# Kernel optimization log

Measured on AMD Instinct MI355X. Metric: run time of the kernel, lower is better.

The kernel has to match this reference:

```python
import jax, jax.numpy as jnp
import numpy as np

B, C, NC, H, W = 8, 128, 19, 128, 256
EPS = 1e-5


def ste_round(x):
    # straight-through-estimator round (Brevitas-style)
    return x + jax.lax.stop_gradient(jnp.round(x) - x)


def quant_weight(w):
    # int4 symmetric per-output-channel fake-quant: levels [-7, 7]
    s = jnp.maximum(jnp.max(jnp.abs(w), axis=(1, 2, 3), keepdims=True) / 7.0, 1e-8)
    wq = jnp.clip(ste_round(w / s), -7.0, 7.0) * s
    return wq, s


def quant_relu(x, s):
    # ReLU + uint4 fake-quant with learned per-tensor scale: levels [0, 15]
    return jnp.clip(ste_round(x / s), 0.0, 15.0) * s


def batchnorm(x, g, b, m, v):
    scale = (g / jnp.sqrt(v + EPS))[None, :, None, None]
    return (x - m[None, :, None, None]) * scale + b[None, :, None, None]


def dwconv3x3(x, w):
    # w: [C,1,3,3], groups=C
    return jax.lax.conv_general_dilated(
        x, w, window_strides=(1, 1), padding=((1, 1), (1, 1)),
        dimension_numbers=('NCHW', 'OIHW', 'NCHW'),
        feature_group_count=x.shape[1])


def pwconv(x, w):
    # 1x1 conv as einsum; w: [O,I,1,1]
    return jnp.einsum('bchw,oc->bohw', x, w[:, :, 0, 0])


def dsconv(x, dw_w, bn1, s1, pw_w, bn2, s2):
    wq, _ = quant_weight(dw_w)
    x = dwconv3x3(x, wq)
    x = batchnorm(x, *bn1)
    x = quant_relu(x, s1)
    wq, _ = quant_weight(pw_w)
    x = pwconv(x, wq)
    x = batchnorm(x, *bn2)
    x = quant_relu(x, s2)
    return x


def setup_inputs() -> dict:
    key = jax.random.key(0)
    ks = jax.random.split(key, 16)
    d = {}
    d['x'] = jax.random.normal(ks[0], (B, C, H, W), dtype=jnp.float32)
    d['dw1_w'] = jax.random.normal(ks[1], (C, 1, 3, 3), dtype=jnp.float32) * 0.1
    d['pw1_w'] = jax.random.normal(ks[2], (C, C, 1, 1), dtype=jnp.float32) * 0.05
    d['dw2_w'] = jax.random.normal(ks[3], (C, 1, 3, 3), dtype=jnp.float32) * 0.1
    d['pw2_w'] = jax.random.normal(ks[4], (C, C, 1, 1), dtype=jnp.float32) * 0.05
    d['cls_w'] = jax.random.normal(ks[5], (NC, C, 1, 1), dtype=jnp.float32) * 0.05
    d['cls_b'] = jax.random.normal(ks[6], (NC,), dtype=jnp.float32) * 0.1
    for i, kk in zip(range(1, 5), ks[7:11]):
        sub = jax.random.split(kk, 4)
        d[f'bn{i}_g'] = 1.0 + 0.1 * jax.random.normal(sub[0], (C,), dtype=jnp.float32)
        d[f'bn{i}_b'] = 0.1 * jax.random.normal(sub[1], (C,), dtype=jnp.float32)
        d[f'bn{i}_m'] = 0.1 * jax.random.normal(sub[2], (C,), dtype=jnp.float32)
        d[f'bn{i}_v'] = jax.random.uniform(sub[3], (C,), dtype=jnp.float32, minval=0.5, maxval=1.5)
    d['s_a1'] = jnp.float32(0.2)
    d['s_a2'] = jnp.float32(0.2)
    d['s_a3'] = jnp.float32(0.2)
    d['s_a4'] = jnp.float32(0.2)
    return d


def reference(x, dw1_w, pw1_w, dw2_w, pw2_w, cls_w, cls_b,
              bn1_g, bn1_b, bn1_m, bn1_v,
              bn2_g, bn2_b, bn2_m, bn2_v,
              bn3_g, bn3_b, bn3_m, bn3_v,
              bn4_g, bn4_b, bn4_m, bn4_v,
              s_a1, s_a2, s_a3, s_a4):
    x = dsconv(x, dw1_w, (bn1_g, bn1_b, bn1_m, bn1_v), s_a1,
               pw1_w, (bn2_g, bn2_b, bn2_m, bn2_v), s_a2)
    x = dsconv(x, dw2_w, (bn3_g, bn3_b, bn3_m, bn3_v), s_a3,
               pw2_w, (bn4_g, bn4_b, bn4_m, bn4_v), s_a4)
    # QuantDropout p=0.1 is identity in eval mode
    wq, sw = quant_weight(cls_w)
    # IntBias: bias quantized with scale = act_scale * weight_scale (per out channel)
    sb = s_a4 * sw[:, 0, 0, 0]
    bq = ste_round(cls_b / sb) * sb
    out = pwconv(x, wq) + bq[None, :, None, None]
    return out
```

## Files before the change

kernel.cpp:

```cpp
#include <hip/hip_runtime.h>

typedef __attribute__((ext_vector_type(4))) float f32x4;
typedef __attribute__((ext_vector_type(8))) short bf16x8;
typedef __attribute__((ext_vector_type(2))) unsigned int u32x2;
typedef __attribute__((ext_vector_type(4))) unsigned int u32x4;

#define EPSV 1e-5f

#define OFF_BUFA 0u
#define OFF_BUFB 33554432u
#define OFF_T    67108864u
#define OFF_WQ1  (OFF_T + 0u)
#define OFF_R3F  (OFF_T + 6144u)
#define OFF_CST3 (OFF_T + 10752u)
#define OFF_CST1 (OFF_T + 12800u)
#define OFF_R2BF (OFF_T + 14848u)
#define OFF_CST2 (OFF_T + 47616u)
#define OFF_R4BF (OFF_T + 49664u)
#define OFF_CST4 (OFF_T + 82432u)
#define OFF_R5BF (OFF_T + 84480u)
#define OFF_CST5 (OFF_T + 92672u)

struct PArgs {
  const float *dw1, *pw1, *dw2, *pw2, *clsw, *clsb;
  const float *g1, *b1, *m1, *v1;
  const float *g2, *b2, *m2, *v2;
  const float *g3, *b3, *m3, *v3;
  const float *g4, *b4, *m4, *v4;
  const float *s1, *s2, *s3, *s4;
};

__device__ __forceinline__ unsigned short f2bf(float f) {
  return (unsigned short)(__builtin_bit_cast(unsigned int, f) >> 16);
}
__device__ __forceinline__ float clip7(float r) { return fminf(fmaxf(r, -7.f), 7.f); }

__device__ __forceinline__ unsigned int qstep(float a, f32x4 c, float s) {
  float t = (a * c.x - c.z) * c.y + c.w;
  float u = t / s;
  float k = fminf(fmaxf(rintf(u), 0.f), 15.f);
  return (unsigned int)k;
}

__device__ __forceinline__ void cvt2(unsigned int d, unsigned int &lo, unsigned int &hi) {
  float f0 = (float)(d & 0xffu);
  float f1 = (float)((d >> 8) & 0xffu);
  float f2 = (float)((d >> 16) & 0xffu);
  float f3 = (float)(d >> 24);
  lo = (__builtin_bit_cast(unsigned int, f0) >> 16) | (__builtin_bit_cast(unsigned int, f1) & 0xffff0000u);
  hi = (__builtin_bit_cast(unsigned int, f2) >> 16) | (__builtin_bit_cast(unsigned int, f3) & 0xffff0000u);
}

__device__ __forceinline__ float wmax16(float v) {
  #pragma unroll
  for (int s = 1; s < 16; s <<= 1) v = fmaxf(v, __shfl_xor(v, s));
  return v;
}
__device__ __forceinline__ float wmax64(float v) {
  #pragma unroll
  for (int s = 1; s < 64; s <<= 1) v = fmaxf(v, __shfl_xor(v, s));
  return v;
}

__global__ __launch_bounds__(64) void prep_kernel(PArgs P, char* __restrict__ ws) {
  int bi = blockIdx.x, l = threadIdx.x;
  float* wq1 = (float*)(ws + OFF_WQ1);
  float* r3f = (float*)(ws + OFF_R3F);
  f32x4* cst1 = (f32x4*)(ws + OFF_CST1);
  f32x4* cst2 = (f32x4*)(ws + OFF_CST2);
  f32x4* cst3 = (f32x4*)(ws + OFF_CST3);
  f32x4* cst4 = (f32x4*)(ws + OFF_CST4);
  unsigned short* r2 = (unsigned short*)(ws + OFF_R2BF);
  unsigned short* r4 = (unsigned short*)(ws + OFF_R4BF);
  unsigned short* r5 = (unsigned short*)(ws + OFF_R5BF);
  float2* cst5 = (float2*)(ws + OFF_CST5);

  if (bi < 128) {
    int c = bi;
    float w = (l < 9) ? P.dw1[c * 9 + l] : 0.f;
    float mx = wmax16(fabsf(w));
    float sq = fmaxf(mx / 7.0f, 1e-8f);
    if (l < 9) wq1[c * 12 + l] = clip7(rintf(w / sq)) * sq;
    if (l == 0) {
      float sc = P.g1[c] / sqrtf(P.v1[c] + EPSV);
      cst1[c] = f32x4{1.f, sc, P.m1[c], P.b1[c]};
    }
  } else if (bi < 256) {
    int o = bi - 128;
    float w0 = P.pw1[o * 128 + l], w1 = P.pw1[o * 128 + 64 + l];
    float mx = wmax64(fmaxf(fabsf(w0), fabsf(w1)));
    float sq = fmaxf(mx / 7.0f, 1e-8f);
    r2[o * 128 + l]      = f2bf(clip7(rintf(w0 / sq)));
    r2[o * 128 + 64 + l] = f2bf(clip7(rintf(w1 / sq)));
    if (l == 0) {
      float sc = P.g2[o] / sqrtf(P.v2[o] + EPSV);
      cst2[o] = f32x4{P.s1[0] * sq, sc, P.m2[o], P.b2[o]};
    }
  } else if (bi < 384) {
    int c = bi - 256;
    float w = (l < 9) ? P.dw2[c * 9 + l] : 0.f;
    float mx = wmax16(fabsf(w));
    float sq = fmaxf(mx / 7.0f, 1e-8f);
    if (l < 9) r3f[l * 128 + c] = clip7(rintf(w / sq));
    if (l == 0) {
      float sc = P.g3[c] / sqrtf(P.v3[c] + EPSV);
      cst3[c] = f32x4{P.s2[0] * sq, sc, P.m3[c], P.b3[c]};
    }
  } else if (bi < 512) {
    int o = bi - 384;
    float w0 = P.pw2[o * 128 + l], w1 = P.pw2[o * 128 + 64 + l];
    float mx = wmax64(fmaxf(fabsf(w0), fabsf(w1)));
    float sq = fmaxf(mx / 7.0f, 1e-8f);
    r4[o * 128 + l]      = f2bf(clip7(rintf(w0 / sq)));
    r4[o * 128 + 64 + l] = f2bf(clip7(rintf(w1 / sq)));
    if (l == 0) {
      float sc = P.g4[o] / sqrtf(P.v4[o] + EPSV);
      cst4[o] = f32x4{P.s3[0] * sq, sc, P.m4[o], P.b4[o]};
    }
  } else {
    int o = bi - 512;
    if (o < 19) {
      float w0 = P.clsw[o * 128 + l], w1 = P.clsw[o * 128 + 64 + l];
      float mx = wmax64(fmaxf(fabsf(w0), fabsf(w1)));
      float sq = fmaxf(mx / 7.0f, 1e-8f);
      r5[o * 128 + l]      = f2bf(clip7(rintf(w0 / sq)));
      r5[o * 128 + 64 + l] = f2bf(clip7(rintf(w1 / sq)));
      if (l == 0) {
        float A5 = P.s4[0] * sq;
        float bq = rintf(P.clsb[o] / A5) * A5;
        cst5[o] = make_float2(A5, bq);
      }
    } else {
      r5[o * 128 + l] = 0; r5[o * 128 + 64 + l] = 0;
      if (l == 0) cst5[o] = make_float2(0.f, 0.f);
    }
  }
}

__global__ __launch_bounds__(512) void dwA_kernel(const float* __restrict__ x,
                                                  char* __restrict__ ws,
                                                  const float* __restrict__ s1p) {
  int bid = blockIdx.x;
  int b = bid & 7, c = bid >> 3;
  int tid = threadIdx.x;
  int wq = tid & 63, wv = tid >> 6;
  int w0 = wq << 2;
  int h0 = wv << 4;
  const float* wp = (const float*)(ws + OFF_WQ1) + c * 12;
  float k0 = wp[0], k1 = wp[1], k2 = wp[2], k3 = wp[3], k4 = wp[4],
        k5 = wp[5], k6 = wp[6], k7 = wp[7], k8 = wp[8];
  f32x4 cs = ((const f32x4*)(ws + OFF_CST1))[c];
  float s_act = *s1p;
  const float* plane = x + (((size_t)((b << 7) | c)) << 15);
  unsigned char* oplane = (unsigned char*)(ws + OFF_BUFB) + (((size_t)((b << 7) | c)) << 15);

  f32x4 vm = {0.f, 0.f, 0.f, 0.f};
  if (h0 > 0) vm = *(const f32x4*)(plane + ((h0 - 1) << 8) + w0);
  f32x4 v0 = *(const f32x4*)(plane + (h0 << 8) + w0);
  f32x4 vp = *(const f32x4*)(plane + ((h0 + 1) << 8) + w0);
  float lm = __shfl_up(vm.w, 1), l0 = __shfl_up(v0.w, 1), lp = __shfl_up(vp.w, 1);
  float rm = __shfl_down(vm.x, 1), r0 = __shfl_down(v0.x, 1), rp = __shfl_down(vp.x, 1);
  if (wq == 0)  { lm = 0.f; l0 = 0.f; lp = 0.f; }
  if (wq == 63) { rm = 0.f; r0 = 0.f; rp = 0.f; }

  #pragma unroll 4
  for (int i = 0; i < 16; i++) {
    int h = h0 + i;
    float y0 = 0.f, y1 = 0.f, y2 = 0.f, y3 = 0.f;
    y0 = fmaf(lm,   k0, y0); y0 = fmaf(vm.x, k1, y0); y0 = fmaf(vm.y, k2, y0);
    y1 = fmaf(vm.x, k0, y1); y1 = fmaf(vm.y, k1, y1); y1 = fmaf(vm.z, k2, y1);
    y2 = fmaf(vm.y, k0, y2); y2 = fmaf(vm.z, k1, y2); y2 = fmaf(vm.w, k2, y2);
    y3 = fmaf(vm.z, k0, y3); y3 = fmaf(vm.w, k1, y3); y3 = fmaf(rm,   k2, y3);

    y0 = fmaf(l0,   k3, y0); y0 = fmaf(v0.x, k4, y0); y0 = fmaf(v0.y, k5, y0);
    y1 = fmaf(v0.x, k3, y1); y1 = fmaf(v0.y, k4, y1); y1 = fmaf(v0.z, k5, y1);
    y2 = fmaf(v0.y, k3, y2); y2 = fmaf(v0.z, k4, y2); y2 = fmaf(v0.w, k5, y2);
    y3 = fmaf(v0.z, k3, y3); y3 = fmaf(v0.w, k4, y3); y3 = fmaf(r0,   k5, y3);

    y0 = fmaf(lp,   k6, y0); y0 = fmaf(vp.x, k7, y0); y0 = fmaf(vp.y, k8, y0);
    y1 = fmaf(vp.x, k6, y1); y1 = fmaf(vp.y, k7, y1); y1 = fmaf(vp.z, k8, y1);
    y2 = fmaf(vp.y, k6, y2); y2 = fmaf(vp.z, k7, y2); y2 = fmaf(vp.w, k8, y2);
    y3 = fmaf(vp.z, k6, y3); y3 = fmaf(vp.w, k7, y3); y3 = fmaf(rp,   k8, y3);

    unsigned int pk = qstep(y0, cs, s_act) | (qstep(y1, cs, s_act) << 8) |
                      (qstep(y2, cs, s_act) << 16) | (qstep(y3, cs, s_act) << 24);
    *(unsigned int*)(oplane + (h << 8) + w0) = pk;

    vm = v0; lm = l0; rm = r0;
    v0 = vp; l0 = lp; r0 = rp;
    f32x4 nv = {0.f, 0.f, 0.f, 0.f};
    if (i < 15 && h + 2 < 128) nv = *(const f32x4*)(plane + ((h + 2) << 8) + w0);
    vp = nv;
    float nl = __shfl_up(nv.w, 1), nr = __shfl_down(nv.x, 1);
    if (wq == 0)  nl = 0.f;
    if (wq == 63) nr = 0.f;
    lp = nl; rp = nr;
  }
}

__global__ __launch_bounds__(256) void pwn_kernel(const unsigned char* __restrict__ in,
                                                  unsigned char* __restrict__ out,
                                                  const unsigned short* __restrict__ rbf,
                                                  const f32x4* __restrict__ cst,
                                                  const float* __restrict__ sp) {
  __shared__ unsigned char lds[32768];
  int tid = threadIdx.x;
  int p0 = blockIdx.x << 7;
  int b_img = p0 >> 15, loc0 = p0 & 32767;
  {
    int pb = tid & 7, cq = tid >> 3;
    int c4 = cq << 2;
    int kc = cq >> 3, lgr = (cq >> 1) & 3, half = cq & 1;
    const unsigned char* ib = in + (((size_t)(b_img << 7)) << 15) + loc0 + (pb << 4);
    u32x4 t0 = *(const u32x4*)(ib + ((size_t)(c4 + 0) << 15));
    u32x4 t1 = *(const u32x4*)(ib + ((size_t)(c4 + 1) << 15));
    u32x4 t2 = *(const u32x4*)(ib + ((size_t)(c4 + 2) << 15));
    u32x4 t3 = *(const u32x4*)(ib + ((size_t)(c4 + 3) << 15));
    int swz = (pb & 7) << 4;
    #pragma unroll
    for (int s = 0; s < 16; s++) {
      int wrd = s >> 2, sh8 = (s & 3) << 3;
      unsigned int chw = ((t0[wrd] >> sh8) & 0xffu)
                       | (((t1[wrd] >> sh8) & 0xffu) << 8)
                       | (((t2[wrd] >> sh8) & 0xffu) << 16)
                       | (((t3[wrd] >> sh8) & 0xffu) << 24);
      unsigned int lo, hi;
      cvt2(chw, lo, hi);
      int ad = ((((((pb << 2) + kc) << 6) | s | (lgr << 4)) << 4) + (half << 3)) ^ swz;
      *(u32x2*)(lds + ad) = u32x2{lo, hi};
    }
  }
  __syncthreads();
  int l = tid & 63, wv = tid >> 6;
  int ob = wv << 5;
  bf16x8 af[2][4];
  #pragma unroll
  for (int ot = 0; ot < 2; ot++)
    #pragma unroll
    for (int kc = 0; kc < 4; kc++) {
      int o = ob + (ot << 4) + (l & 15);
      int k = (kc << 5) + ((l >> 4) << 3);
      af[ot][kc] = *(const bf16x8*)(rbf + o * 128 + k);
    }
  f32x4 acc[2][8];
  #pragma unroll
  for (int ot = 0; ot < 2; ot++)
    #pragma unroll
    for (int pt = 0; pt < 8; pt++) acc[ot][pt] = f32x4{0.f, 0.f, 0.f, 0.f};
  #pragma unroll
  for (int kc = 0; kc < 4; kc++) {
    bf16x8 bb[8];
    #pragma unroll
    for (int pt = 0; pt < 8; pt++)
      bb[pt] = *(const bf16x8*)(lds + (((((((pt << 2) + kc) << 6)) + l) << 4) ^ ((pt & 7) << 4)));
    #pragma unroll
    for (int ot = 0; ot < 2; ot++)
      #pragma unroll
      for (int pt = 0; pt < 8; pt++)
        acc[ot][pt] = __builtin_amdgcn_mfma_f32_16x16x32_bf16(af[ot][kc], bb[pt], acc[ot][pt], 0, 0, 0);
  }
  float s_act = *sp;
  #pragma unroll
  for (int ot = 0; ot < 2; ot++) {
    int o0 = ob + (ot << 4) + ((l >> 4) << 2);
    f32x4 c0 = cst[o0], c1 = cst[o0 + 1], c2 = cst[o0 + 2], c3 = cst[o0 + 3];
    #pragma unroll
    for (int pt = 0; pt < 8; pt++) {
      int p = p0 + (pt << 4) + (l & 15);
      f32x4 a = acc[ot][pt];
      unsigned int pk = qstep(a.x, c0, s_act) | (qstep(a.y, c1, s_act) << 8) |
                        (qstep(a.z, c2, s_act) << 16) | (qstep(a.w, c3, s_act) << 24);
      *(unsigned int*)(out + (size_t)p * 128 + o0) = pk;
    }
  }
}

__global__ __launch_bounds__(256) void dw2_kernel(const unsigned char* __restrict__ in,
                                                  unsigned char* __restrict__ out,
                                                  const char* __restrict__ ws,
                                                  const float* __restrict__ sp) {
  __shared__ float tabs[1664];
  const float* src = (const float*)(ws + OFF_R3F);
  for (int i = threadIdx.x; i < 1664; i += 256) tabs[i] = src[i];
  __syncthreads();
  int tid = threadIdx.x;
  int cq = tid & 31, pg = tid >> 5;
  int c4 = cq << 2;
  float wk[9][4];
  #pragma unroll
  for (int t = 0; t < 9; t++) {
    wk[t][0] = tabs[t * 128 + c4];     wk[t][1] = tabs[t * 128 + c4 + 1];
    wk[t][2] = tabs[t * 128 + c4 + 2]; wk[t][3] = tabs[t * 128 + c4 + 3];
  }
  const f32x4* cst3 = (const f32x4*)(tabs + 1152);
  f32x4 cs0 = cst3[c4], cs1 = cst3[c4 + 1], cs2 = cst3[c4 + 2], cs3 = cst3[c4 + 3];
  float s_act = *sp;
  int pbase = (blockIdx.x << 5) + (pg << 2);
  int wbase = pbase & 255, hh = (pbase >> 8) & 127;

  unsigned int xw[3][6];
  #pragma unroll
  for (int r = 0; r < 3; r++) {
    int dh = r - 1;
    bool rowok = (hh + dh >= 0) && (hh + dh <= 127);
    #pragma unroll
    for (int i = 0; i < 6; i++) {
      int wo = wbase + i - 1;
      unsigned int v = 0;
      if (rowok && wo >= 0 && wo <= 255)
        v = *(const unsigned int*)(in + (size_t)(pbase + dh * 256 + (i - 1)) * 128 + c4);
      xw[r][i] = v;
    }
  }
  #pragma unroll
  for (int j = 0; j < 4; j++) {
    float a0 = 0.f, a1 = 0.f, a2 = 0.f, a3 = 0.f;
    #pragma unroll
    for (int r = 0; r < 3; r++) {
      #pragma unroll
      for (int dwi = 0; dwi < 3; dwi++) {
        unsigned int v = xw[r][j + dwi];
        int t = r * 3 + dwi;
        a0 = fmaf((float)(v & 0xffu),         wk[t][0], a0);
        a1 = fmaf((float)((v >> 8) & 0xffu),  wk[t][1], a1);
        a2 = fmaf((float)((v >> 16) & 0xffu), wk[t][2], a2);
        a3 = fmaf((float)(v >> 24),           wk[t][3], a3);
      }
    }
    unsigned int pk = qstep(a0, cs0, s_act) | (qstep(a1, cs1, s_act) << 8) |
                      (qstep(a2, cs2, s_act) << 16) | (qstep(a3, cs3, s_act) << 24);
    *(unsigned int*)(out + (size_t)(pbase + j) * 128 + c4) = pk;
  }
}

__global__ __launch_bounds__(256) void pwcls_kernel(const unsigned char* __restrict__ in,
                                                    float* __restrict__ out,
                                                    const unsigned short* __restrict__ rbf,
                                                    const f32x4* __restrict__ cst,
                                                    const float* __restrict__ sp,
                                                    const unsigned short* __restrict__ r5,
                                                    const float2* __restrict__ cst5) {
  __shared__ unsigned char lds[32768];
  int tid = threadIdx.x;
  int p0 = blockIdx.x << 7;
  #pragma unroll
  for (int it = 0; it < 4; it++) {
    int idx = tid + (it << 8);
    int p = idx >> 3, q = idx & 7;
    int kc = q >> 1, lg = (q & 1) << 1, pt = p >> 4;
    u32x4 g = *(const u32x4*)(in + (size_t)(p0 + p) * 128 + q * 16);
    unsigned int a0, a1, a2, a3, a4, a5, a6, a7;
    cvt2(g.x, a0, a1); cvt2(g.y, a2, a3); cvt2(g.z, a4, a5); cvt2(g.w, a6, a7);
    int l1 = (p & 15) | (lg << 4);
    int ad = (((((pt << 2) + kc) << 6) | l1) << 4);
    *(u32x4*)(lds + ad)       = u32x4{a0, a1, a2, a3};
    *(u32x4*)(lds + ad + 256) = u32x4{a4, a5, a6, a7};
  }
  __syncthreads();
  int l = tid & 63, wv = tid >> 6;
  int ob = wv << 5;
  bf16x8 af[2][4];
  #pragma unroll
  for (int ot = 0; ot < 2; ot++)
    #pragma unroll
    for (int kc = 0; kc < 4; kc++) {
      int o = ob + (ot << 4) + (l & 15);
      int k = (kc << 5) + ((l >> 4) << 3);
      af[ot][kc] = *(const bf16x8*)(rbf + o * 128 + k);
    }
  f32x4 acc[2][8];
  #pragma unroll
  for (int ot = 0; ot < 2; ot++)
    #pragma unroll
    for (int pt = 0; pt < 8; pt++) acc[ot][pt] = f32x4{0.f, 0.f, 0.f, 0.f};
  #pragma unroll
  for (int kc = 0; kc < 4; kc++) {
    bf16x8 bb[8];
    #pragma unroll
    for (int pt = 0; pt < 8; pt++)
      bb[pt] = *(const bf16x8*)(lds + ((((((pt << 2) + kc) << 6)) + l) << 4));
    #pragma unroll
    for (int ot = 0; ot < 2; ot++)
      #pragma unroll
      for (int pt = 0; pt < 8; pt++)
        acc[ot][pt] = __builtin_amdgcn_mfma_f32_16x16x32_bf16(af[ot][kc], bb[pt], acc[ot][pt], 0, 0, 0);
  }
  float s_act = *sp;
  __syncthreads();
  {
    int hsel = (l >> 4) & 1;
    #pragma unroll
    for (int ot = 0; ot < 2; ot++) {
      int o0 = ob + (ot << 4) + ((l >> 4) << 2);
      f32x4 c0 = cst[o0], c1 = cst[o0 + 1], c2 = cst[o0 + 2], c3 = cst[o0 + 3];
      int hi = (ot << 1) + ((l >> 4) >> 1);
      int lfrag = (l & 15) | (hi << 4);
      #pragma unroll
      for (int pt = 0; pt < 8; pt++) {
        f32x4 a = acc[ot][pt];
        unsigned int k0 = qstep(a.x, c0, s_act), k1 = qstep(a.y, c1, s_act);
        unsigned int k2 = qstep(a.z, c2, s_act), k3 = qstep(a.w, c3, s_act);
        unsigned int w0 = (__builtin_bit_cast(unsigned int, (float)k0) >> 16) |
                          (__builtin_bit_cast(unsigned int, (float)k1) & 0xffff0000u);
        unsigned int w1 = (__builtin_bit_cast(unsigned int, (float)k2) >> 16) |
                          (__builtin_bit_cast(unsigned int, (float)k3) & 0xffff0000u);
        int ad = (((((pt << 2) + wv) << 6) | lfrag) << 4) + (hsel << 3);
        *(u32x2*)(lds + ad) = u32x2{w0, w1};
      }
    }
  }
  __syncthreads();
  int pt0 = wv << 1;
  bf16x8 af5[2][4];
  #pragma unroll
  for (int ot = 0; ot < 2; ot++)
    #pragma unroll
    for (int kc = 0; kc < 4; kc++) {
      int o = (ot << 4) + (l & 15);
      int k = (kc << 5) + ((l >> 4) << 3);
      af5[ot][kc] = *(const bf16x8*)(r5 + o * 128 + k);
    }
  f32x4 a5[2][2] = {{{0,0,0,0},{0,0,0,0}},{{0,0,0,0},{0,0,0,0}}};
  #pragma unroll
  for (int kc = 0; kc < 4; kc++) {
    bf16x8 b0 = *(const bf16x8*)(lds + ((((((pt0    ) << 2) + kc) << 6) + l) << 4));
    bf16x8 b1 = *(const bf16x8*)(lds + ((((((pt0 + 1) << 2) + kc) << 6) + l) << 4));
    #pragma unroll
    for (int ot = 0; ot < 2; ot++) {
      a5[ot][0] = __builtin_amdgcn_mfma_f32_16x16x32_bf16(af5[ot][kc], b0, a5[ot][0], 0, 0, 0);
      a5[ot][1] = __builtin_amdgcn_mfma_f32_16x16x32_bf16(af5[ot][kc], b1, a5[ot][1], 0, 0, 0);
    }
  }
  #pragma unroll
  for (int ptl = 0; ptl < 2; ptl++) {
    int p = p0 + ((pt0 + ptl) << 4) + (l & 15);
    int bb = p >> 15, hw = p & 32767;
    float* ob2 = out + (((size_t)bb * 19) << 15) + hw;
    #pragma unroll
    for (int ot = 0; ot < 2; ot++) {
      int obase = (ot << 4) + ((l >> 4) << 2);
      f32x4 a = a5[ot][ptl];
      #pragma unroll
      for (int i = 0; i < 4; i++) {
        int o = obase + i;
        if (o < 19) {
          float2 c5 = cst5[o];
          ob2[(size_t)o << 15] = fmaf(a[i], c5.x, c5.y);
        }
      }
    }
  }
}

extern "C" void kernel_launch(void* const* d_in, const int* in_sizes, int n_in,
                              void* d_out, int out_size, void* d_ws, size_t ws_size,
                              hipStream_t stream) {
  (void)in_sizes; (void)n_in; (void)out_size; (void)ws_size;
  char* ws = (char*)d_ws;
  PArgs P;
  P.dw1  = (const float*)d_in[1];
  P.pw1  = (const float*)d_in[2];
  P.dw2  = (const float*)d_in[3];
  P.pw2  = (const float*)d_in[4];
  P.clsw = (const float*)d_in[5];
  P.clsb = (const float*)d_in[6];
  P.g1 = (const float*)d_in[7];  P.b1 = (const float*)d_in[8];
  P.m1 = (const float*)d_in[9];  P.v1 = (const float*)d_in[10];
  P.g2 = (const float*)d_in[11]; P.b2 = (const float*)d_in[12];
  P.m2 = (const float*)d_in[13]; P.v2 = (const float*)d_in[14];
  P.g3 = (const float*)d_in[15]; P.b3 = (const float*)d_in[16];
  P.m3 = (const float*)d_in[17]; P.v3 = (const float*)d_in[18];
  P.g4 = (const float*)d_in[19]; P.b4 = (const float*)d_in[20];
  P.m4 = (const float*)d_in[21]; P.v4 = (const float*)d_in[22];
  P.s1 = (const float*)d_in[23]; P.s2 = (const float*)d_in[24];
  P.s3 = (const float*)d_in[25]; P.s4 = (const float*)d_in[26];

  const float* x = (const float*)d_in[0];
  unsigned char* bufA = (unsigned char*)(ws + OFF_BUFA);
  unsigned char* bufB = (unsigned char*)(ws + OFF_BUFB);

  prep_kernel<<<544, 64, 0, stream>>>(P, ws);
  dwA_kernel<<<1024, 512, 0, stream>>>(x, ws, P.s1);
  pwn_kernel<<<2048, 256, 0, stream>>>(bufB, bufA,
      (const unsigned short*)(ws + OFF_R2BF), (const f32x4*)(ws + OFF_CST2), P.s2);
  dw2_kernel<<<8192, 256, 0, stream>>>(bufA, bufB, ws, P.s3);
  pwcls_kernel<<<2048, 256, 0, stream>>>(bufB, (float*)d_out,
      (const unsigned short*)(ws + OFF_R4BF), (const f32x4*)(ws + OFF_CST4), P.s4,
      (const unsigned short*)(ws + OFF_R5BF), (const float2*)(ws + OFF_CST5));
}
```

Measured before the change: 136.4 us.

## Fuse second depthwise conv into pointwise+classifier kernel via swizzled LDS

Merges the second depthwise 3x3 kernel into the following pointwise+classifier kernel. Each block now computes dw2 for its 128 pixels and writes quantized bf16 values straight into the MFMA operand layout in LDS. This removes the uint8 intermediate write and re-read through global memory and one kernel launch. An XOR swizzle on the LDS slot index is added to avoid bank conflicts. Per-block work grows, dw weights are read from global memory rather than LDS, and the halo rows are reloaded by each block.

```diff
diff --git a/kernel.cpp b/kernel.cpp
--- a/kernel.cpp
+++ b/kernel.cpp
@@ -35,11 +35,13 @@
 }
 __device__ __forceinline__ float clip7(float r) { return fminf(fmaxf(r, -7.f), 7.f); }
 
-__device__ __forceinline__ unsigned int qstep(float a, f32x4 c, float s) {
+__device__ __forceinline__ float qstepf(float a, f32x4 c, float s) {
   float t = (a * c.x - c.z) * c.y + c.w;
   float u = t / s;
-  float k = fminf(fmaxf(rintf(u), 0.f), 15.f);
-  return (unsigned int)k;
+  return fminf(fmaxf(rintf(u), 0.f), 15.f);
+}
+__device__ __forceinline__ unsigned int qstep(float a, f32x4 c, float s) {
+  return (unsigned int)qstepf(a, c, s);
 }
 
 __device__ __forceinline__ void cvt2(unsigned int d, unsigned int &lo, unsigned int &hi) {
@@ -275,86 +277,78 @@
   }
 }
 
-__global__ __launch_bounds__(256) void dw2_kernel(const unsigned char* __restrict__ in,
-                                                  unsigned char* __restrict__ out,
-                                                  const char* __restrict__ ws,
-                                                  const float* __restrict__ sp) {
-  __shared__ float tabs[1664];
-  const float* src = (const float*)(ws + OFF_R3F);
-  for (int i = threadIdx.x; i < 1664; i += 256) tabs[i] = src[i];
-  __syncthreads();
-  int tid = threadIdx.x;
-  int cq = tid & 31, pg = tid >> 5;
-  int c4 = cq << 2;
-  float wk[9][4];
-  #pragma unroll
-  for (int t = 0; t < 9; t++) {
-    wk[t][0] = tabs[t * 128 + c4];     wk[t][1] = tabs[t * 128 + c4 + 1];
-    wk[t][2] = tabs[t * 128 + c4 + 2]; wk[t][3] = tabs[t * 128 + c4 + 3];
-  }
-  const f32x4* cst3 = (const f32x4*)(tabs + 1152);
-  f32x4 cs0 = cst3[c4], cs1 = cst3[c4 + 1], cs2 = cst3[c4 + 2], cs3 = cst3[c4 + 3];
-  float s_act = *sp;
-  int pbase = (blockIdx.x << 5) + (pg << 2);
-  int wbase = pbase & 255, hh = (pbase >> 8) & 127;
-
-  unsigned int xw[3][6];
-  #pragma unroll
-  for (int r = 0; r < 3; r++) {
-    int dh = r - 1;
-    bool rowok = (hh + dh >= 0) && (hh + dh <= 127);
-    #pragma unroll
-    for (int i = 0; i < 6; i++) {
-      int wo = wbase + i - 1;
-      unsigned int v = 0;
-      if (rowok && wo >= 0 && wo <= 255)
-        v = *(const unsigned int*)(in + (size_t)(pbase + dh * 256 + (i - 1)) * 128 + c4);
-      xw[r][i] = v;
-    }
-  }
-  #pragma unroll
-  for (int j = 0; j < 4; j++) {
-    float a0 = 0.f, a1 = 0.f, a2 = 0.f, a3 = 0.f;
-    #pragma unroll
-    for (int r = 0; r < 3; r++) {
-      #pragma unroll
-      for (int dwi = 0; dwi < 3; dwi++) {
-        unsigned int v = xw[r][j + dwi];
-        int t = r * 3 + dwi;
-        a0 = fmaf((float)(v & 0xffu),         wk[t][0], a0);
-        a1 = fmaf((float)((v >> 8) & 0xffu),  wk[t][1], a1);
-        a2 = fmaf((float)((v >> 16) & 0xffu), wk[t][2], a2);
-        a3 = fmaf((float)(v >> 24),           wk[t][3], a3);
-      }
-    }
-    unsigned int pk = qstep(a0, cs0, s_act) | (qstep(a1, cs1, s_act) << 8) |
-                      (qstep(a2, cs2, s_act) << 16) | (qstep(a3, cs3, s_act) << 24);
-    *(unsigned int*)(out + (size_t)(pbase + j) * 128 + c4) = pk;
-  }
-}
-
-__global__ __launch_bounds__(256) void pwcls_kernel(const unsigned char* __restrict__ in,
-                                                    float* __restrict__ out,
-                                                    const unsigned short* __restrict__ rbf,
-                                                    const f32x4* __restrict__ cst,
-                                                    const float* __restrict__ sp,
-                                                    const unsigned short* __restrict__ r5,
-                                                    const float2* __restrict__ cst5) {
+__global__ __launch_bounds__(256) void dw2pwcls_kernel(const unsigned char* __restrict__ in,
+                                                       float* __restrict__ out,
+                                                       const char* __restrict__ ws,
+                                                       const unsigned short* __restrict__ rbf,
+                                                       const f32x4* __restrict__ cst,
+                                                       const float* __restrict__ s3p,
+                                                       const float* __restrict__ s4p,
+                                                       const unsigned short* __restrict__ r5,
+                                                       const float2* __restrict__ cst5) {
   __shared__ unsigned char lds[32768];
   int tid = threadIdx.x;
   int p0 = blockIdx.x << 7;
-  #pragma unroll
-  for (int it = 0; it < 4; it++) {
-    int idx = tid + (it << 8);
-    int p = idx >> 3, q = idx & 7;
-    int kc = q >> 1, lg = (q & 1) << 1, pt = p >> 4;
-    u32x4 g = *(const u32x4*)(in + (size_t)(p0 + p) * 128 + q * 16);
-    unsigned int a0, a1, a2, a3, a4, a5, a6, a7;
-    cvt2(g.x, a0, a1); cvt2(g.y, a2, a3); cvt2(g.z, a4, a5); cvt2(g.w, a6, a7);
-    int l1 = (p & 15) | (lg << 4);
-    int ad = (((((pt << 2) + kc) << 6) | l1) << 4);
-    *(u32x4*)(lds + ad)       = u32x4{a0, a1, a2, a3};
-    *(u32x4*)(lds + ad + 256) = u32x4{a4, a5, a6, a7};
+  {
+    int cq = tid & 31, pg = tid >> 5;
+    int c4 = cq << 2;
+    const float* r3f = (const float*)(ws + OFF_R3F);
+    float wk[9][4];
+    #pragma unroll
+    for (int t = 0; t < 9; t++) {
+      wk[t][0] = r3f[t * 128 + c4];     wk[t][1] = r3f[t * 128 + c4 + 1];
+      wk[t][2] = r3f[t * 128 + c4 + 2]; wk[t][3] = r3f[t * 128 + c4 + 3];
+    }
+    const f32x4* cst3 = (const f32x4*)(ws + OFF_CST3);
+    f32x4 cs0 = cst3[c4], cs1 = cst3[c4 + 1], cs2 = cst3[c4 + 2], cs3 = cst3[c4 + 3];
+    float s_act3 = *s3p;
+    int kc = c4 >> 5, hi = (c4 >> 3) & 3, half = (c4 >> 2) & 1;
+    int g = hi | ((kc & 1) << 2);
+    for (int ps = 0; ps < 4; ps++) {
+      int pbase = p0 + (ps << 5) + (pg << 2);
+      int wbase = pbase & 255, hh = (pbase >> 8) & 127;
+      unsigned int xw[3][6];
+      #pragma unroll
+      for (int r = 0; r < 3; r++) {
+        int dh = r - 1;
+        bool rowok = (hh + dh >= 0) && (hh + dh <= 127);
+        #pragma unroll
+        for (int i = 0; i < 6; i++) {
+          int wo = wbase + i - 1;
+          unsigned int v = 0;
+          if (rowok && wo >= 0 && wo <= 255)
+            v = *(const unsigned int*)(in + (size_t)(pbase + dh * 256 + (i - 1)) * 128 + c4);
+          xw[r][i] = v;
+        }
+      }
+      #pragma unroll
+      for (int j = 0; j < 4; j++) {
+        float a0 = 0.f, a1 = 0.f, a2 = 0.f, a3 = 0.f;
+        #pragma unroll
+        for (int r = 0; r < 3; r++) {
+          #pragma unroll
+          for (int dwi = 0; dwi < 3; dwi++) {
+            unsigned int v = xw[r][j + dwi];
+            int t = r * 3 + dwi;
+            a0 = fmaf((float)(v & 0xffu),         wk[t][0], a0);
+            a1 = fmaf((float)((v >> 8) & 0xffu),  wk[t][1], a1);
+            a2 = fmaf((float)((v >> 16) & 0xffu), wk[t][2], a2);
+            a3 = fmaf((float)(v >> 24),           wk[t][3], a3);
+          }
+        }
+        float k0f = qstepf(a0, cs0, s_act3), k1f = qstepf(a1, cs1, s_act3);
+        float k2f = qstepf(a2, cs2, s_act3), k3f = qstepf(a3, cs3, s_act3);
+        unsigned int wlo = (__builtin_bit_cast(unsigned int, k0f) >> 16) |
+                           (__builtin_bit_cast(unsigned int, k1f) & 0xffff0000u);
+        unsigned int whi = (__builtin_bit_cast(unsigned int, k2f) >> 16) |
+                           (__builtin_bit_cast(unsigned int, k3f) & 0xffff0000u);
+        int p_local = (ps << 5) + (pg << 2) + j;
+        int pt = p_local >> 4, pl = p_local & 15;
+        int slot = (pl ^ g) | (hi << 4);
+        int ad = (((((pt << 2) + kc) << 6) | slot) << 4) + (half << 3);
+        *(u32x2*)(lds + ad) = u32x2{wlo, whi};
+      }
+    }
   }
   __syncthreads();
   int l = tid & 63, wv = tid >> 6;
@@ -375,17 +369,18 @@
     for (int pt = 0; pt < 8; pt++) acc[ot][pt] = f32x4{0.f, 0.f, 0.f, 0.f};
   #pragma unroll
   for (int kc = 0; kc < 4; kc++) {
+    int gg = (l >> 4) | ((kc & 1) << 2);
     bf16x8 bb[8];
     #pragma unroll
     for (int pt = 0; pt < 8; pt++)
-      bb[pt] = *(const bf16x8*)(lds + ((((((pt << 2) + kc) << 6)) + l) << 4));
+      bb[pt] = *(const bf16x8*)(lds + ((((((pt << 2) + kc) << 6)) | (l ^ gg)) << 4));
     #pragma unroll
     for (int ot = 0; ot < 2; ot++)
       #pragma unroll
       for (int pt = 0; pt < 8; pt++)
         acc[ot][pt] = __builtin_amdgcn_mfma_f32_16x16x32_bf16(af[ot][kc], bb[pt], acc[ot][pt], 0, 0, 0);
   }
-  float s_act = *sp;
+  float s_act4 = *s4p;
   __syncthreads();
   {
     int hsel = (l >> 4) & 1;
@@ -398,12 +393,12 @@
       #pragma unroll
       for (int pt = 0; pt < 8; pt++) {
         f32x4 a = acc[ot][pt];
-        unsigned int k0 = qstep(a.x, c0, s_act), k1 = qstep(a.y, c1, s_act);
-        unsigned int k2 = qstep(a.z, c2, s_act), k3 = qstep(a.w, c3, s_act);
-        unsigned int w0 = (__builtin_bit_cast(unsigned int, (float)k0) >> 16) |
-                          (__builtin_bit_cast(unsigned int, (float)k1) & 0xffff0000u);
-        unsigned int w1 = (__builtin_bit_cast(unsigned int, (float)k2) >> 16) |
-                          (__builtin_bit_cast(unsigned int, (float)k3) & 0xffff0000u);
+        float k0f = qstepf(a.x, c0, s_act4), k1f = qstepf(a.y, c1, s_act4);
+        float k2f = qstepf(a.z, c2, s_act4), k3f = qstepf(a.w, c3, s_act4);
+        unsigned int w0 = (__builtin_bit_cast(unsigned int, k0f) >> 16) |
+                          (__builtin_bit_cast(unsigned int, k1f) & 0xffff0000u);
+        unsigned int w1 = (__builtin_bit_cast(unsigned int, k2f) >> 16) |
+                          (__builtin_bit_cast(unsigned int, k3f) & 0xffff0000u);
         int ad = (((((pt << 2) + wv) << 6) | lfrag) << 4) + (hsel << 3);
         *(u32x2*)(lds + ad) = u32x2{w0, w1};
       }
@@ -483,8 +478,8 @@
   dwA_kernel<<<1024, 512, 0, stream>>>(x, ws, P.s1);
   pwn_kernel<<<2048, 256, 0, stream>>>(bufB, bufA,
       (const unsigned short*)(ws + OFF_R2BF), (const f32x4*)(ws + OFF_CST2), P.s2);
-  dw2_kernel<<<8192, 256, 0, stream>>>(bufA, bufB, ws, P.s3);
-  pwcls_kernel<<<2048, 256, 0, stream>>>(bufB, (float*)d_out,
-      (const unsigned short*)(ws + OFF_R4BF), (const f32x4*)(ws + OFF_CST4), P.s4,
+  dw2pwcls_kernel<<<2048, 256, 0, stream>>>(bufA, (float*)d_out, ws,
+      (const unsigned short*)(ws + OFF_R4BF), (const f32x4*)(ws + OFF_CST4),
+      P.s3, P.s4,
       (const unsigned short*)(ws + OFF_R5BF), (const float2*)(ws + OFF_CST5));
 }
```

Measured after the change: 136.1 us. Within noise of the previous version (-0.2%).
